# Kernel optimization log

Hardware: AMD Instinct MI355X
Metric: run time of the kernel (lower is better)

Reference implementation:

```python
import jax, jax.numpy as jnp
import numpy as np

NUM_HEADS = 4
C_IN = 80   # in_channels[0] (raw camera BEV channels)
C = 126     # in_channels[1]
D = C + 2   # 128, inner attention dim


def _conv(x, w, b=None):
    # NCHW conv, 3x3, SAME padding (padding=1)
    y = jax.lax.conv_general_dilated(x, w, (1, 1), 'SAME',
                                     dimension_numbers=('NCHW', 'OIHW', 'NCHW'))
    if b is not None:
        y = y + b[None, :, None, None]
    return y


def setup_inputs() -> dict:
    key = jax.random.key(0)
    ks = jax.random.split(key, 16)
    s = 0.02
    inp = {
        'lidar_bev': jax.random.normal(ks[0], (1, C, 64, 64), jnp.float32),
        'cam_bev': jax.random.normal(ks[1], (1, C_IN, 64, 64), jnp.float32),
        'cam_enc_w': jax.random.normal(ks[2], (C, C_IN, 3, 3), jnp.float32) * s,
        'cam_enc_b': jnp.zeros((C,), jnp.float32),
        'cam_v_w': jax.random.normal(ks[3], (D, C), jnp.float32) * s,
        'cam_qk_w': jax.random.normal(ks[4], (2 * D, C), jnp.float32) * s,
        'cam_proj_w': jax.random.normal(ks[5], (C, D), jnp.float32) * s,
        'cam_proj_b': jnp.zeros((C,), jnp.float32),
        'lidar_v_w': jax.random.normal(ks[6], (D, C), jnp.float32) * s,
        'lidar_qk_w': jax.random.normal(ks[7], (2 * D, C), jnp.float32) * s,
        'lidar_proj_w': jax.random.normal(ks[8], (C, D), jnp.float32) * s,
        'lidar_proj_b': jnp.zeros((C,), jnp.float32),
        'fuser_w': jax.random.normal(ks[9], (C, 4 * C, 3, 3), jnp.float32) * s,
    }
    return inp


def reference(lidar_bev, cam_bev, cam_enc_w, cam_enc_b, cam_v_w, cam_qk_w,
              cam_proj_w, cam_proj_b, lidar_v_w, lidar_qk_w, lidar_proj_w,
              lidar_proj_b, fuser_w):
    B, Cc, H, W = lidar_bev.shape
    N = H * W
    nh, hd = NUM_HEADS, D // NUM_HEADS
    scale = Cc ** (-0.5)  # in_channels[1] ** -0.5

    cam_enc = _conv(cam_bev, cam_enc_w, cam_enc_b)  # [B,C,H,W] (SCNET stand-in)

    cam_f = cam_enc.reshape(B, Cc, N).transpose(0, 2, 1)     # [B,N,C]
    lid_f = lidar_bev.reshape(B, Cc, N).transpose(0, 2, 1)    # [B,N,C]

    def heads(x):  # [B,N,D] -> [B,nh,N,hd]
        return x.reshape(B, N, nh, hd).transpose(0, 2, 1, 3)

    cam_v = heads(cam_f @ cam_v_w.T)
    lid_v = heads(lid_f @ lidar_v_w.T)

    def qk(x, w):  # -> (q, k) each [B,nh,N,hd]
        t = (x @ w.T).reshape(B, N, 2, nh, hd).transpose(2, 0, 3, 1, 4)
        return t[0], t[1]

    lid_q, lid_k = qk(lid_f, lidar_qk_w)
    cam_q, cam_k = qk(cam_f, cam_qk_w)

    def merge(o):  # [B,nh,N,hd] -> [B,N,D]
        return o.transpose(0, 2, 1, 3).reshape(B, N, D)

    def to_map(x):  # [B,N,C] -> [B,C,H,W]
        return x.reshape(B, H, W, Cc).transpose(0, 3, 1, 2)

    # lidar-driven attention, reused against two value tensors
    lid_attn = jax.nn.softmax(jnp.einsum('bhnd,bhmd->bhnm', lid_q, lid_k) * scale, axis=-1)
    cam_by_lid = to_map(merge(lid_attn @ cam_v) @ cam_proj_w.T + cam_proj_b)
    cam_bev_l = cam_enc + cam_by_lid
    lid_by_lid = to_map(merge(lid_attn @ lid_v) @ lidar_proj_w.T + lidar_proj_b)
    lidar_bev_l = lidar_bev + lid_by_lid

    # camera-driven attention (note: original code uses lidar_proj for BOTH outputs here)
    cam_attn = jax.nn.softmax(jnp.einsum('bhnd,bhmd->bhnm', cam_q, cam_k) * scale, axis=-1)
    cam_by_cam = to_map(merge(cam_attn @ cam_v) @ lidar_proj_w.T + lidar_proj_b)
    cam_bev_c = cam_enc + cam_by_cam
    lid_by_cam = to_map(merge(cam_attn @ lid_v) @ lidar_proj_w.T + lidar_proj_b)
    lidar_bev_c = lidar_bev + lid_by_cam

    fused_in = jnp.concatenate([cam_bev_c, cam_bev_l, lidar_bev_c, lidar_bev_l], axis=1)
    return _conv(fused_in, fuser_w)
```

## Files before the change

kernel.cpp:

```cpp
#include <hip/hip_runtime.h>
#include <hip/hip_bf16.h>

typedef unsigned short ushort_t;
using f32x4  = __attribute__((ext_vector_type(4))) float;
using f32x16 = __attribute__((ext_vector_type(16))) float;
using bf16x8 = __attribute__((ext_vector_type(8))) short;
typedef unsigned uint2v __attribute__((ext_vector_type(2)));

#define N_PIX 4096

static __device__ __forceinline__ unsigned short f2bf(float f) {
  unsigned int u = __builtin_bit_cast(unsigned int, f);
  u += 0x7FFFu + ((u >> 16) & 1u);
  return (unsigned short)(u >> 16);
}
static __device__ __forceinline__ float bf2f(unsigned int us) {
  return __builtin_bit_cast(float, us << 16);
}

typedef union {
  uint4 u4;
  unsigned u[4];
  unsigned long long q[2];
  bf16x8 v;
  unsigned short us[8];
} fragU;

#define LDS_U32(p) ((unsigned)(uintptr_t)((__attribute__((address_space(3))) void*)(p)))

__global__ __launch_bounds__(256) void zero_span_k(uint4* __restrict__ p, int n16) {
  int i = blockIdx.x * 256 + threadIdx.x;
  if (i < n16) p[i] = (uint4){0u, 0u, 0u, 0u};
}

__global__ __launch_bounds__(256) void prep_k(
    const float* __restrict__ cam_enc_w, const float* __restrict__ fuser_w,
    const float* __restrict__ lid_proj_w, const float* __restrict__ cam_proj_w,
    const float* __restrict__ lid_qk_w, const float* __restrict__ cam_qk_w,
    const float* __restrict__ cam_v_w, const float* __restrict__ lid_v_w,
    const float* __restrict__ cam_bev, const float* __restrict__ lidar_bev,
    ushort_t* __restrict__ Wp_c, ushort_t* __restrict__ Wp_f,
    ushort_t* __restrict__ Wp_lid, ushort_t* __restrict__ Wp_cam,
    ushort_t* __restrict__ Wq,
    ushort_t* __restrict__ cm, ushort_t* __restrict__ ch_,
    ushort_t* __restrict__ lidBF) {
  const float QSCALE = 0.08908708063747479f * 1.4426950408889634f;
  int idx = blockIdx.x * 256 + threadIdx.x;
  if (idx < 110592) {
    int kk = idx / 12288, r = idx % 12288;
    int co = r / 96, ci = r % 96;
    float v = (co < 126 && ci < 80) ? cam_enc_w[(co * 80 + ci) * 9 + kk] : 0.f;
    Wp_c[idx] = f2bf(v);
  } else if (idx < 700416) {
    int j = idx - 110592;
    int kk = j / 65536, r = j % 65536;
    int co = r / 512, ci = r % 512;
    float v = (co < 126 && ci < 504) ? fuser_w[(co * 504 + ci) * 9 + kk] : 0.f;
    Wp_f[j] = f2bf(v);
  } else if (idx < 716800) {
    int j = idx - 700416;
    int co = j >> 7, k = j & 127;
    Wp_lid[j] = f2bf(co < 126 ? lid_proj_w[co * 128 + k] : 0.f);
  } else if (idx < 733184) {
    int j = idx - 716800;
    int co = j >> 7, k = j & 127;
    Wp_cam[j] = f2bf(co < 126 ? cam_proj_w[co * 128 + k] : 0.f);
  } else if (idx < 831488) {
    int j = idx - 733184;
    int t = j >> 14, r = j & 16383;
    int row = r >> 7, ci = r & 127;
    float v = 0.f;
    if (ci < 126) {
      if (t == 0)      v = lid_qk_w[row * 126 + ci] * QSCALE;
      else if (t == 1) v = lid_qk_w[(128 + row) * 126 + ci];
      else if (t == 2) v = cam_qk_w[row * 126 + ci] * QSCALE;
      else if (t == 3) v = cam_qk_w[(128 + row) * 126 + ci];
      else if (t == 4) v = cam_v_w[row * 126 + ci];
      else             v = lid_v_w[row * 126 + ci];
    }
    Wq[j] = f2bf(v);
  } else {
    int k = idx - 831488;
    if (k < 327680) {
      int ch = k >> 12, n = k & 4095;
      int y = n >> 6, x = n & 63;
      unsigned short b = f2bf(cam_bev[k]);
      cm[ch * 4224 + (y + 1) * 64 + x] = b;
      ch_[ch * 4356 + (y + 1) * 66 + (x + 1)] = b;
    } else {
      int j = k - 327680;
      if (j < 516096) lidBF[j] = f2bf(lidar_bev[j]);
    }
  }
}

__global__ __launch_bounds__(256) void conv_mfma_k(
    const ushort_t* __restrict__ Amain,
    const ushort_t* __restrict__ Ahalo,
    const ushort_t* __restrict__ Wp,
    ushort_t* __restrict__ parts,
    int CIp, int ksteps) {
  __shared__ __align__(16) ushort_t Abuf[2][2048];
  const int y   = blockIdx.x;
  const int kk  = blockIdx.y;
  const int ky  = kk / 3, kx = kk - ky * 3;
  const int tid = threadIdx.x;
  const int w   = tid >> 6, l = tid & 63;
  const int lane15 = l & 15, g = l >> 4;
  const int yy1 = y + ky;

  const int ci_l = w * 8 + (l >> 5) * 4 + ((l & 7) >> 1);
  const int m0   = ((l >> 3) & 3) * 16 + (l & 1) * 8;
  const ushort_t* src;
  size_t plane;
  if (kx == 1) { plane = 66 * 64; src = Amain + (size_t)ci_l * plane + yy1 * 64 + m0; }
  else         { plane = 66 * 66; src = Ahalo + (size_t)ci_l * plane + yy1 * 66 + m0 + kx; }

  const ushort_t* wbase = Wp + ((size_t)kk * 128 + w * 32 + lane15) * CIp + g * 8;
  const unsigned tr_base = LDS_U32(&Abuf[0][0]) + (unsigned)(g * 1024 + lane15 * 8);

  f32x4 acc[4][2];
  #pragma unroll
  for (int q = 0; q < 4; ++q) {
    acc[q][0] = (f32x4){0.f, 0.f, 0.f, 0.f};
    acc[q][1] = (f32x4){0.f, 0.f, 0.f, 0.f};
  }

  __builtin_amdgcn_global_load_lds(
      (const __attribute__((address_space(1))) unsigned*)src,
      (__attribute__((address_space(3))) unsigned*)(&Abuf[0][w * 512]), 16, 0, 0);
  __syncthreads();

  for (int s = 0; s < ksteps; ++s) {
    if (s + 1 < ksteps) {
      const ushort_t* srcn = src + (size_t)(s + 1) * 32 * plane;
      __builtin_amdgcn_global_load_lds(
          (const __attribute__((address_space(1))) unsigned*)srcn,
          (__attribute__((address_space(3))) unsigned*)(&Abuf[(s + 1) & 1][w * 512]), 16, 0, 0);
    }
    const ushort_t* wb = wbase + s * 32;
    fragU fb0, fb1;
    fb0.u4 = *(const uint4*)(wb);
    fb1.u4 = *(const uint4*)(wb + 16 * CIp);

    unsigned ta = tr_base + (unsigned)((s & 1) << 12);
    unsigned long long r00, r01, r10, r11, r20, r21, r30, r31;
    asm volatile("ds_read_b64_tr_b16 %0, %1 offset:0"   : "=v"(r00) : "v"(ta));
    asm volatile("ds_read_b64_tr_b16 %0, %1 offset:512" : "=v"(r01) : "v"(ta));
    asm volatile("ds_read_b64_tr_b16 %0, %1 offset:128" : "=v"(r10) : "v"(ta));
    asm volatile("ds_read_b64_tr_b16 %0, %1 offset:640" : "=v"(r11) : "v"(ta));
    asm volatile("ds_read_b64_tr_b16 %0, %1 offset:256" : "=v"(r20) : "v"(ta));
    asm volatile("ds_read_b64_tr_b16 %0, %1 offset:768" : "=v"(r21) : "v"(ta));
    asm volatile("ds_read_b64_tr_b16 %0, %1 offset:384" : "=v"(r30) : "v"(ta));
    asm volatile("ds_read_b64_tr_b16 %0, %1 offset:896" : "=v"(r31) : "v"(ta));
    asm volatile("s_waitcnt lgkmcnt(0)" ::: "memory");
    __builtin_amdgcn_sched_barrier(0);

    fragU fa;
    fa.q[0] = r00; fa.q[1] = r01;
    acc[0][0] = __builtin_amdgcn_mfma_f32_16x16x32_bf16(fa.v, fb0.v, acc[0][0], 0, 0, 0);
    acc[0][1] = __builtin_amdgcn_mfma_f32_16x16x32_bf16(fa.v, fb1.v, acc[0][1], 0, 0, 0);
    fa.q[0] = r10; fa.q[1] = r11;
    acc[1][0] = __builtin_amdgcn_mfma_f32_16x16x32_bf16(fa.v, fb0.v, acc[1][0], 0, 0, 0);
    acc[1][1] = __builtin_amdgcn_mfma_f32_16x16x32_bf16(fa.v, fb1.v, acc[1][1], 0, 0, 0);
    fa.q[0] = r20; fa.q[1] = r21;
    acc[2][0] = __builtin_amdgcn_mfma_f32_16x16x32_bf16(fa.v, fb0.v, acc[2][0], 0, 0, 0);
    acc[2][1] = __builtin_amdgcn_mfma_f32_16x16x32_bf16(fa.v, fb1.v, acc[2][1], 0, 0, 0);
    fa.q[0] = r30; fa.q[1] = r31;
    acc[3][0] = __builtin_amdgcn_mfma_f32_16x16x32_bf16(fa.v, fb0.v, acc[3][0], 0, 0, 0);
    acc[3][1] = __builtin_amdgcn_mfma_f32_16x16x32_bf16(fa.v, fb1.v, acc[3][1], 0, 0, 0);
    __syncthreads();
  }

  ushort_t* pout = parts + (size_t)kk * 524288 + (size_t)(w * 32 + lane15) * 4096
                 + y * 64 + g * 4;
  #pragma unroll
  for (int q = 0; q < 4; ++q) {
    ushort4 p0, p1;
    p0.x = f2bf(acc[q][0][0]); p0.y = f2bf(acc[q][0][1]);
    p0.z = f2bf(acc[q][0][2]); p0.w = f2bf(acc[q][0][3]);
    p1.x = f2bf(acc[q][1][0]); p1.y = f2bf(acc[q][1][1]);
    p1.z = f2bf(acc[q][1][2]); p1.w = f2bf(acc[q][1][3]);
    *(ushort4*)(pout + q * 16)             = p0;
    *(ushort4*)(pout + 16 * 4096 + q * 16) = p1;
  }
}

__global__ __launch_bounds__(256) void reduce9_k(
    const ushort_t* __restrict__ parts, float* __restrict__ out,
    ushort_t* __restrict__ outbf, const float* __restrict__ bias) {
  int n0 = (blockIdx.x * 256 + threadIdx.x) * 8;
  int co = blockIdx.y;
  size_t off = (size_t)co * 4096 + n0;
  float s[8] = {0, 0, 0, 0, 0, 0, 0, 0};
  #pragma unroll
  for (int kk = 0; kk < 9; ++kk) {
    uint4 v = *(const uint4*)(parts + (size_t)kk * 524288 + off);
    s[0] += bf2f(v.x & 0xffffu); s[1] += bf2f(v.x >> 16);
    s[2] += bf2f(v.y & 0xffffu); s[3] += bf2f(v.y >> 16);
    s[4] += bf2f(v.z & 0xffffu); s[5] += bf2f(v.z >> 16);
    s[6] += bf2f(v.w & 0xffffu); s[7] += bf2f(v.w >> 16);
  }
  float b = bias ? bias[co] : 0.f;
  #pragma unroll
  for (int i = 0; i < 8; ++i) s[i] += b;
  if (out) {
    f32x4 o0 = {s[0], s[1], s[2], s[3]};
    f32x4 o1 = {s[4], s[5], s[6], s[7]};
    *(f32x4*)(out + off)     = o0;
    *(f32x4*)(out + off + 4) = o1;
  }
  if (outbf) {
    ushort4 b0, b1;
    b0.x = f2bf(s[0]); b0.y = f2bf(s[1]); b0.z = f2bf(s[2]); b0.w = f2bf(s[3]);
    b1.x = f2bf(s[4]); b1.y = f2bf(s[5]); b1.z = f2bf(s[6]); b1.w = f2bf(s[7]);
    *(ushort4*)(outbf + off)     = b0;
    *(ushort4*)(outbf + off + 4) = b1;
  }
}

__global__ __launch_bounds__(256) void qkv_mfma_k(
    const ushort_t* __restrict__ lidBF, const ushort_t* __restrict__ camBF,
    const ushort_t* __restrict__ Wq,
    ushort_t* __restrict__ lidQK, ushort_t* __restrict__ camQK,
    ushort_t* __restrict__ camV, ushort_t* __restrict__ lidV) {
  __shared__ __align__(16) ushort_t Abuf[2][2048];
  const int y = blockIdx.x, t = blockIdx.y;
  const ushort_t* X = (t >= 2 && t <= 4) ? camBF : lidBF;
  const int tid = threadIdx.x;
  const int w = tid >> 6, l = tid & 63;
  const int lane15 = l & 15, g = l >> 4;
  const int ci_l = w * 8 + (l >> 5) * 4 + ((l & 7) >> 1);
  const int m0   = ((l >> 3) & 3) * 16 + (l & 1) * 8;
  const ushort_t* src = X + (size_t)ci_l * 4096 + y * 64 + m0;
  const ushort_t* wbase = Wq + (size_t)t * 16384 + (w * 32 + lane15) * 128 + g * 8;
  const unsigned tr_base = LDS_U32(&Abuf[0][0]) + (unsigned)(g * 1024 + lane15 * 8);

  f32x4 acc[4][2];
  #pragma unroll
  for (int q = 0; q < 4; ++q) {
    acc[q][0] = (f32x4){0.f, 0.f, 0.f, 0.f};
    acc[q][1] = (f32x4){0.f, 0.f, 0.f, 0.f};
  }

  __builtin_amdgcn_global_load_lds(
      (const __attribute__((address_space(1))) unsigned*)src,
      (__attribute__((address_space(3))) unsigned*)(&Abuf[0][w * 512]), 16, 0, 0);
  __syncthreads();

  for (int s = 0; s < 4; ++s) {
    if (s < 3) {
      const ushort_t* srcn = src + (size_t)(s + 1) * 32 * 4096;
      __builtin_amdgcn_global_load_lds(
          (const __attribute__((address_space(1))) unsigned*)srcn,
          (__attribute__((address_space(3))) unsigned*)(&Abuf[(s + 1) & 1][w * 512]), 16, 0, 0);
    }
    const ushort_t* wb = wbase + s * 32;
    fragU fb0, fb1;
    fb0.u4 = *(const uint4*)(wb);
    fb1.u4 = *(const uint4*)(wb + 16 * 128);

    unsigned ta = tr_base + (unsigned)((s & 1) << 12);
    unsigned long long r00, r01, r10, r11, r20, r21, r30, r31;
    asm volatile("ds_read_b64_tr_b16 %0, %1 offset:0"   : "=v"(r00) : "v"(ta));
    asm volatile("ds_read_b64_tr_b16 %0, %1 offset:512" : "=v"(r01) : "v"(ta));
    asm volatile("ds_read_b64_tr_b16 %0, %1 offset:128" : "=v"(r10) : "v"(ta));
    asm volatile("ds_read_b64_tr_b16 %0, %1 offset:640" : "=v"(r11) : "v"(ta));
    asm volatile("ds_read_b64_tr_b16 %0, %1 offset:256" : "=v"(r20) : "v"(ta));
    asm volatile("ds_read_b64_tr_b16 %0, %1 offset:768" : "=v"(r21) : "v"(ta));
    asm volatile("ds_read_b64_tr_b16 %0, %1 offset:384" : "=v"(r30) : "v"(ta));
    asm volatile("ds_read_b64_tr_b16 %0, %1 offset:896" : "=v"(r31) : "v"(ta));
    asm volatile("s_waitcnt lgkmcnt(0)" ::: "memory");
    __builtin_amdgcn_sched_barrier(0);

    fragU fa;
    fa.q[0] = r00; fa.q[1] = r01;
    acc[0][0] = __builtin_amdgcn_mfma_f32_16x16x32_bf16(fa.v, fb0.v, acc[0][0], 0, 0, 0);
    acc[0][1] = __builtin_amdgcn_mfma_f32_16x16x32_bf16(fa.v, fb1.v, acc[0][1], 0, 0, 0);
    fa.q[0] = r10; fa.q[1] = r11;
    acc[1][0] = __builtin_amdgcn_mfma_f32_16x16x32_bf16(fa.v, fb0.v, acc[1][0], 0, 0, 0);
    acc[1][1] = __builtin_amdgcn_mfma_f32_16x16x32_bf16(fa.v, fb1.v, acc[1][1], 0, 0, 0);
    fa.q[0] = r20; fa.q[1] = r21;
    acc[2][0] = __builtin_amdgcn_mfma_f32_16x16x32_bf16(fa.v, fb0.v, acc[2][0], 0, 0, 0);
    acc[2][1] = __builtin_amdgcn_mfma_f32_16x16x32_bf16(fa.v, fb1.v, acc[2][1], 0, 0, 0);
    fa.q[0] = r30; fa.q[1] = r31;
    acc[3][0] = __builtin_amdgcn_mfma_f32_16x16x32_bf16(fa.v, fb0.v, acc[3][0], 0, 0, 0);
    acc[3][1] = __builtin_amdgcn_mfma_f32_16x16x32_bf16(fa.v, fb1.v, acc[3][1], 0, 0, 0);
    __syncthreads();
  }

  if (t < 4) {
    ushort_t* dst = (t < 2) ? lidQK : camQK;
    const int colbase = (t & 1) * 128 + w * 32 + lane15;
    #pragma unroll
    for (int q = 0; q < 4; ++q)
      #pragma unroll
      for (int tt = 0; tt < 2; ++tt)
        #pragma unroll
        for (int r = 0; r < 4; ++r) {
          int n = y * 64 + q * 16 + g * 4 + r;
          dst[(size_t)n * 256 + colbase + tt * 16] = f2bf(acc[q][tt][r]);
        }
  } else {
    ushort_t* dst = (t == 4) ? camV : lidV;
    ushort_t* pout = dst + (size_t)(w * 32 + lane15) * 4096 + y * 64 + g * 4;
    #pragma unroll
    for (int q = 0; q < 4; ++q) {
      ushort4 p0, p1;
      p0.x = f2bf(acc[q][0][0]); p0.y = f2bf(acc[q][0][1]);
      p0.z = f2bf(acc[q][0][2]); p0.w = f2bf(acc[q][0][3]);
      p1.x = f2bf(acc[q][1][0]); p1.y = f2bf(acc[q][1][1]);
      p1.z = f2bf(acc[q][1][2]); p1.w = f2bf(acc[q][1][3]);
      *(ushort4*)(pout + q * 16)             = p0;
      *(ushort4*)(pout + 16 * 4096 + q * 16) = p1;
    }
  }
}

__global__ __launch_bounds__(256) void flash_attn_mfma(
    const ushort_t* __restrict__ lidQK, const ushort_t* __restrict__ camQK,
    const ushort_t* __restrict__ camV, const ushort_t* __restrict__ lidV,
    ushort_t* __restrict__ OP, float2* __restrict__ ML) {
  const int i0    = blockIdx.x * 128;
  const int h     = blockIdx.y;
  const int attn  = blockIdx.z >> 1;
  const int half  = blockIdx.z & 1;
  const int kbase = half * 2048;
  const ushort_t* QK = attn ? camQK : lidQK;

  __shared__ __align__(16) ushort_t Ks[2][64 * 40];
  __shared__ __align__(16) ushort_t Vt[2][64 * 72];

  const int tid = threadIdx.x;
  const int w = tid >> 6, l = tid & 63;
  const int q31 = l & 31, hi = l >> 5;
  const int q0w = i0 + w * 32;

  const int srow = tid >> 2, sc = tid & 3;
  const ushort_t* Kg = QK + (size_t)(kbase + srow) * 256 + 128 + h * 32 + sc * 8;
  const ushort_t* Vg = ((srow >> 5) ? lidV : camV)
                     + (size_t)(h * 32 + (srow & 31)) * N_PIX + kbase;

  fragU qf0, qf1;
  qf0.u4 = *(const uint4*)(QK + (size_t)(q0w + q31) * 256 + h * 32 + hi * 8);
  qf1.u4 = *(const uint4*)(QK + (size_t)(q0w + q31) * 256 + h * 32 + 16 + hi * 8);

  {
    uint4 k4 = *(const uint4*)Kg;
    uint4 va = *(const uint4*)(Vg + sc * 8);
    uint4 vb = *(const uint4*)(Vg + (sc + 4) * 8);
    *(uint4*)(&Ks[0][srow * 40 + sc * 8]) = k4;
    *(uint4*)(&Vt[0][srow * 72 + sc * 8]) = va;
    *(uint4*)(&Vt[0][srow * 72 + (sc + 4) * 8]) = vb;
  }
  __syncthreads();

  fragU ones;
  #pragma unroll
  for (int j = 0; j < 8; ++j) ones.us[j] = 0x3F80;

  f32x16 Oc = (f32x16)0.f, Ol = (f32x16)0.f, lacc = (f32x16)0.f;
  const f32x16 z16 = (f32x16)0.f;

  for (int it = 0; it < 32; ++it) {
    const int cur = it & 1, nxt = cur ^ 1;
    const bool more = (it + 1) < 32;
    uint4 kn, van, vbn;
    if (more) {
      kn  = *(const uint4*)(Kg + (size_t)(it + 1) * 16384);
      van = *(const uint4*)(Vg + (it + 1) * 64 + sc * 8);
      vbn = *(const uint4*)(Vg + (it + 1) * 64 + (sc + 4) * 8);
    }

    const ushort_t* kb = &Ks[cur][0];
    fragU k00, k01, k10, k11;
    k00.u4 = *(const uint4*)(kb + q31 * 40 + hi * 8);
    k01.u4 = *(const uint4*)(kb + q31 * 40 + 16 + hi * 8);
    k10.u4 = *(const uint4*)(kb + (32 + q31) * 40 + hi * 8);
    k11.u4 = *(const uint4*)(kb + (32 + q31) * 40 + 16 + hi * 8);
    f32x16 S0, S1;
    __builtin_amdgcn_s_setprio(1);
    S0 = __builtin_amdgcn_mfma_f32_32x32x16_bf16(k00.v, qf0.v, z16, 0, 0, 0);
    S0 = __builtin_amdgcn_mfma_f32_32x32x16_bf16(k01.v, qf1.v, S0, 0, 0, 0);
    S1 = __builtin_amdgcn_mfma_f32_32x32x16_bf16(k10.v, qf0.v, z16, 0, 0, 0);
    S1 = __builtin_amdgcn_mfma_f32_32x32x16_bf16(k11.v, qf1.v, S1, 0, 0, 0);
    __builtin_amdgcn_s_setprio(0);

    #pragma unroll
    for (int j = 0; j < 16; ++j) S0[j] = __builtin_amdgcn_exp2f(S0[j]);
    #pragma unroll
    for (int j = 0; j < 16; ++j) S1[j] = __builtin_amdgcn_exp2f(S1[j]);

    fragU pa0, pa1, pa2, pa3;
    {
      unsigned a0, a1, b0, b1;
      asm("v_cvt_pk_bf16_f32 %0, %1, %2" : "=v"(a0) : "v"(S0[0]),  "v"(S0[1]));
      asm("v_cvt_pk_bf16_f32 %0, %1, %2" : "=v"(a1) : "v"(S0[2]),  "v"(S0[3]));
      asm("v_cvt_pk_bf16_f32 %0, %1, %2" : "=v"(b0) : "v"(S0[4]),  "v"(S0[5]));
      asm("v_cvt_pk_bf16_f32 %0, %1, %2" : "=v"(b1) : "v"(S0[6]),  "v"(S0[7]));
      uint2v r0 = __builtin_amdgcn_permlane32_swap(a0, b0, false, false);
      uint2v r1 = __builtin_amdgcn_permlane32_swap(a1, b1, false, false);
      pa0.u[0] = r0[0]; pa0.u[1] = r1[0]; pa0.u[2] = r0[1]; pa0.u[3] = r1[1];
      asm("v_cvt_pk_bf16_f32 %0, %1, %2" : "=v"(a0) : "v"(S0[8]),  "v"(S0[9]));
      asm("v_cvt_pk_bf16_f32 %0, %1, %2" : "=v"(a1) : "v"(S0[10]), "v"(S0[11]));
      asm("v_cvt_pk_bf16_f32 %0, %1, %2" : "=v"(b0) : "v"(S0[12]), "v"(S0[13]));
      asm("v_cvt_pk_bf16_f32 %0, %1, %2" : "=v"(b1) : "v"(S0[14]), "v"(S0[15]));
      r0 = __builtin_amdgcn_permlane32_swap(a0, b0, false, false);
      r1 = __builtin_amdgcn_permlane32_swap(a1, b1, false, false);
      pa1.u[0] = r0[0]; pa1.u[1] = r1[0]; pa1.u[2] = r0[1]; pa1.u[3] = r1[1];
      asm("v_cvt_pk_bf16_f32 %0, %1, %2" : "=v"(a0) : "v"(S1[0]),  "v"(S1[1]));
      asm("v_cvt_pk_bf16_f32 %0, %1, %2" : "=v"(a1) : "v"(S1[2]),  "v"(S1[3]));
      asm("v_cvt_pk_bf16_f32 %0, %1, %2" : "=v"(b0) : "v"(S1[4]),  "v"(S1[5]));
      asm("v_cvt_pk_bf16_f32 %0, %1, %2" : "=v"(b1) : "v"(S1[6]),  "v"(S1[7]));
      r0 = __builtin_amdgcn_permlane32_swap(a0, b0, false, false);
      r1 = __builtin_amdgcn_permlane32_swap(a1, b1, false, false);
      pa2.u[0] = r0[0]; pa2.u[1] = r1[0]; pa2.u[2] = r0[1]; pa2.u[3] = r1[1];
      asm("v_cvt_pk_bf16_f32 %0, %1, %2" : "=v"(a0) : "v"(S1[8]),  "v"(S1[9]));
      asm("v_cvt_pk_bf16_f32 %0, %1, %2" : "=v"(a1) : "v"(S1[10]), "v"(S1[11]));
      asm("v_cvt_pk_bf16_f32 %0, %1, %2" : "=v"(b0) : "v"(S1[12]), "v"(S1[13]));
      asm("v_cvt_pk_bf16_f32 %0, %1, %2" : "=v"(b1) : "v"(S1[14]), "v"(S1[15]));
      r0 = __builtin_amdgcn_permlane32_swap(a0, b0, false, false);
      r1 = __builtin_amdgcn_permlane32_swap(a1, b1, false, false);
      pa3.u[0] = r0[0]; pa3.u[1] = r1[0]; pa3.u[2] = r0[1]; pa3.u[3] = r1[1];
    }

    const ushort_t* vb = &Vt[cur][0];
    __builtin_amdgcn_s_setprio(1);
    {
      fragU vc, vl;
      vc.u4 = *(const uint4*)(vb + q31 * 72 + hi * 8);
      vl.u4 = *(const uint4*)(vb + (32 + q31) * 72 + hi * 8);
      Oc = __builtin_amdgcn_mfma_f32_32x32x16_bf16(pa0.v, vc.v, Oc, 0, 0, 0);
      Ol = __builtin_amdgcn_mfma_f32_32x32x16_bf16(pa0.v, vl.v, Ol, 0, 0, 0);
      lacc = __builtin_amdgcn_mfma_f32_32x32x16_bf16(pa0.v, ones.v, lacc, 0, 0, 0);
      vc.u4 = *(const uint4*)(vb + q31 * 72 + 16 + hi * 8);
      vl.u4 = *(const uint4*)(vb + (32 + q31) * 72 + 16 + hi * 8);
      Oc = __builtin_amdgcn_mfma_f32_32x32x16_bf16(pa1.v, vc.v, Oc, 0, 0, 0);
      Ol = __builtin_amdgcn_mfma_f32_32x32x16_bf16(pa1.v, vl.v, Ol, 0, 0, 0);
      lacc = __builtin_amdgcn_mfma_f32_32x32x16_bf16(pa1.v, ones.v, lacc, 0, 0, 0);
      vc.u4 = *(const uint4*)(vb + q31 * 72 + 32 + hi * 8);
      vl.u4 = *(const uint4*)(vb + (32 + q31) * 72 + 32 + hi * 8);
      Oc = __builtin_amdgcn_mfma_f32_32x32x16_bf16(pa2.v, vc.v, Oc, 0, 0, 0);
      Ol = __builtin_amdgcn_mfma_f32_32x32x16_bf16(pa2.v, vl.v, Ol, 0, 0, 0);
      lacc = __builtin_amdgcn_mfma_f32_32x32x16_bf16(pa2.v, ones.v, lacc, 0, 0, 0);
      vc.u4 = *(const uint4*)(vb + q31 * 72 + 48 + hi * 8);
      vl.u4 = *(const uint4*)(vb + (32 + q31) * 72 + 48 + hi * 8);
      Oc = __builtin_amdgcn_mfma_f32_32x32x16_bf16(pa3.v, vc.v, Oc, 0, 0, 0);
      Ol = __builtin_amdgcn_mfma_f32_32x32x16_bf16(pa3.v, vl.v, Ol, 0, 0, 0);
      lacc = __builtin_amdgcn_mfma_f32_32x32x16_bf16(pa3.v, ones.v, lacc, 0, 0, 0);
    }
    __builtin_amdgcn_s_setprio(0);

    if (more) {
      *(uint4*)(&Ks[nxt][srow * 40 + sc * 8]) = kn;
      *(uint4*)(&Vt[nxt][srow * 72 + sc * 8]) = van;
      *(uint4*)(&Vt[nxt][srow * 72 + (sc + 4) * 8]) = vbn;
    }
    __syncthreads();
  }

  ushort_t* OPc = OP + (size_t)((attn * 2 + half) * 2 + 0) * 4096 * 128;
  ushort_t* OPl = OP + (size_t)((attn * 2 + half) * 2 + 1) * 4096 * 128;
  const int d = h * 32 + q31;
  #pragma unroll
  for (int reg = 0; reg < 16; ++reg) {
    int n = q0w + (reg & 3) + 8 * (reg >> 2) + 4 * hi;
    OPc[(size_t)n * 128 + d] = f2bf(Oc[reg]);
    OPl[(size_t)n * 128 + d] = f2bf(Ol[reg]);
  }
  if (q31 == 0) {
    #pragma unroll
    for (int reg = 0; reg < 16; ++reg) {
      int n = q0w + (reg & 3) + 8 * (reg >> 2) + 4 * hi;
      float2 v; v.x = 0.f; v.y = lacc[reg];
      ML[(size_t)(attn * 2 + half) * 4096 + n] = v;
    }
  }
}

__global__ __launch_bounds__(256) void proj_mfma_k(
    const ushort_t* __restrict__ OP, const float2* __restrict__ ML,
    const ushort_t* __restrict__ Wlid, const ushort_t* __restrict__ Wcam,
    const ushort_t* __restrict__ camBF, const ushort_t* __restrict__ lidBF,
    const float* __restrict__ cam_proj_b, const float* __restrict__ lid_proj_b,
    ushort_t* __restrict__ fm, ushort_t* __restrict__ fh) {
  const int n0 = blockIdx.x * 64;
  const int ot = blockIdx.y;
  const int attn = (ot == 0 || ot == 2) ? 1 : 0;
  const int vt = ot >> 1;
  const int tid = threadIdx.x;
  const int w = tid >> 6, l = tid & 63;
  const int m = l & 15, g = l >> 4;

  const ushort_t* Oa = OP + (size_t)((attn * 2 + 0) * 2 + vt) * 4096 * 128;
  const ushort_t* Ob = OP + (size_t)((attn * 2 + 1) * 2 + vt) * 4096 * 128;
  const float2* MLa = ML + (size_t)(attn * 2 + 0) * 4096;
  const float2* MLb = ML + (size_t)(attn * 2 + 1) * 4096;

  const int arow = n0 + w * 16 + m;
  float2 mla = MLa[arow], mlb = MLb[arow];
  float inv = 1.0f / (mla.y + mlb.y);

  fragU afr[4];
  #pragma unroll
  for (int s = 0; s < 4; ++s) {
    fragU xa, xb;
    xa.u4 = *(const uint4*)(Oa + (size_t)arow * 128 + s * 32 + g * 8);
    xb.u4 = *(const uint4*)(Ob + (size_t)arow * 128 + s * 32 + g * 8);
    #pragma unroll
    for (int j = 0; j < 8; ++j)
      afr[s].us[j] = f2bf(inv * (bf2f(xa.us[j]) + bf2f(xb.us[j])));
  }

  const ushort_t* W = (ot == 1) ? Wcam : Wlid;
  f32x4 acc[8];
  #pragma unroll
  for (int t = 0; t < 8; ++t) acc[t] = (f32x4){0.f, 0.f, 0.f, 0.f};
  #pragma unroll
  for (int s = 0; s < 4; ++s) {
    #pragma unroll
    for (int t = 0; t < 8; ++t) {
      fragU bfr;
      bfr.u4 = *(const uint4*)(W + (size_t)(t * 16 + m) * 128 + s * 32 + g * 8);
      acc[t] = __builtin_amdgcn_mfma_f32_16x16x32_bf16(afr[s].v, bfr.v, acc[t], 0, 0, 0);
    }
  }

  const float* bias = (ot == 1) ? cam_proj_b : lid_proj_b;
  const ushort_t* resBF = (ot < 2) ? camBF : lidBF;
  const int doff = ot * 126;
  #pragma unroll
  for (int t = 0; t < 8; ++t) {
    int co = t * 16 + m;
    if (co < 126) {
      float b = bias[co];
      #pragma unroll
      for (int r = 0; r < 4; ++r) {
        int n = n0 + w * 16 + g * 4 + r;
        float res = bf2f(resBF[(size_t)co * N_PIX + n]);
        float v = acc[t][r] + res + b;
        unsigned short bf = f2bf(v);
        int y = n >> 6, x = n & 63;
        fm[(doff + co) * 4224 + (y + 1) * 64 + x]      = bf;
        fh[(doff + co) * 4356 + (y + 1) * 66 + x + 1]  = bf;
      }
    }
  }
}

extern "C" void kernel_launch(void* const* d_in, const int* in_sizes, int n_in,
                              void* d_out, int out_size, void* d_ws, size_t ws_size,
                              hipStream_t stream) {
  (void)in_sizes; (void)n_in; (void)out_size; (void)ws_size;
  const float* lidar_bev  = (const float*)d_in[0];
  const float* cam_bev    = (const float*)d_in[1];
  const float* cam_enc_w  = (const float*)d_in[2];
  const float* cam_enc_b  = (const float*)d_in[3];
  const float* cam_v_w    = (const float*)d_in[4];
  const float* cam_qk_w   = (const float*)d_in[5];
  const float* cam_proj_w = (const float*)d_in[6];
  const float* cam_proj_b = (const float*)d_in[7];
  const float* lid_v_w    = (const float*)d_in[8];
  const float* lid_qk_w   = (const float*)d_in[9];
  const float* lid_proj_w = (const float*)d_in[10];
  const float* lid_proj_b = (const float*)d_in[11];
  const float* fuser_w    = (const float*)d_in[12];
  float* out = (float*)d_out;

  char* p = (char*)d_ws;
  ushort_t* arena = (ushort_t*)p;
  ushort_t* OP    = (ushort_t*)p;
  float2*   ML    = (float2*)(p + 8388608);
  ushort_t* lidQK = (ushort_t*)(p + 9437184);
  ushort_t* camQK = (ushort_t*)(p + 11534336);
  ushort_t* camV  = (ushort_t*)(p + 13631488);
  ushort_t* lidV  = (ushort_t*)(p + 14680064);
  ushort_t* Wp_c    = (ushort_t*)(p + 17793024);
  ushort_t* Wp_f    = (ushort_t*)(p + 18014208);
  ushort_t* Wp_lid  = (ushort_t*)(p + 19193856);
  ushort_t* Wp_cam  = (ushort_t*)(p + 19226624);
  ushort_t* Wq      = (ushort_t*)(p + 19259392);
  ushort_t* lidBF   = (ushort_t*)(p + 19456000);
  ushort_t* camBF   = (ushort_t*)(p + 20504576);
  ushort_t* camBF_m = (ushort_t*)(p + 21553152);
  ushort_t* camBF_h = (ushort_t*)(p + 22364160);
  ushort_t* fusBF_m = (ushort_t*)(p + 23200512);
  ushort_t* fusBF_h = (ushort_t*)(p + 27525888);

  zero_span_k<<<2548, 256, 0, stream>>>((uint4*)(p + 21553152), 652080);
  prep_k<<<6544, 256, 0, stream>>>(cam_enc_w, fuser_w, lid_proj_w, cam_proj_w,
                                   lid_qk_w, cam_qk_w, cam_v_w, lid_v_w,
                                   cam_bev, lidar_bev,
                                   Wp_c, Wp_f, Wp_lid, Wp_cam, Wq,
                                   camBF_m, camBF_h, lidBF);

  conv_mfma_k<<<dim3(64, 9), 256, 0, stream>>>(camBF_m, camBF_h, Wp_c, arena, 96, 3);
  reduce9_k<<<dim3(2, 126), 256, 0, stream>>>(arena, nullptr, camBF, cam_enc_b);

  qkv_mfma_k<<<dim3(64, 6), 256, 0, stream>>>(lidBF, camBF, Wq, lidQK, camQK, camV, lidV);
  flash_attn_mfma<<<dim3(32, 4, 4), 256, 0, stream>>>(lidQK, camQK, camV, lidV, OP, ML);
  proj_mfma_k<<<dim3(64, 4), 256, 0, stream>>>(OP, ML, Wp_lid, Wp_cam, camBF, lidBF,
                                               cam_proj_b, lid_proj_b, fusBF_m, fusBF_h);

  conv_mfma_k<<<dim3(64, 9), 256, 0, stream>>>(fusBF_m, fusBF_h, Wp_f, arena, 512, 16);
  reduce9_k<<<dim3(2, 126), 256, 0, stream>>>(arena, out, nullptr, nullptr);
}
```

Before: 114.1 us.

## Split attention key range four ways to double flash-attention grid parallelism

The flash attention kernel now splits the key dimension into four chunks instead of two, launching 1024 blocks instead of 512, each iterating half as many key tiles. Partial outputs are placed in workspace regions that overlap the fuser-input buffers, so zeroing of that span is moved to after attention, and the projection kernel sums four partials and four row sums. This aims to raise CU occupancy on the attention stage, at the cost of extra partial-output traffic, a second zeroing launch, and more reduction work in the projection.

```diff
diff --git a/kernel.cpp b/kernel.cpp
--- a/kernel.cpp
+++ b/kernel.cpp
@@ -27,6 +27,11 @@
 } fragU;
 
 #define LDS_U32(p) ((unsigned)(uintptr_t)((__attribute__((address_space(3))) void*)(p)))
+
+static __device__ __forceinline__ size_t op_off(int s) {
+  return (s < 9) ? ((size_t)s << 20) : ((size_t)23200512u + ((size_t)(s - 9) << 20));
+}
+#define ML_OFF 15728640u
 
 __global__ __launch_bounds__(256) void zero_span_k(uint4* __restrict__ p, int n16) {
   int i = blockIdx.x * 256 + threadIdx.x;
@@ -320,12 +325,13 @@
 __global__ __launch_bounds__(256) void flash_attn_mfma(
     const ushort_t* __restrict__ lidQK, const ushort_t* __restrict__ camQK,
     const ushort_t* __restrict__ camV, const ushort_t* __restrict__ lidV,
-    ushort_t* __restrict__ OP, float2* __restrict__ ML) {
+    char* __restrict__ ws) {
   const int i0    = blockIdx.x * 128;
   const int h     = blockIdx.y;
-  const int attn  = blockIdx.z >> 1;
-  const int half  = blockIdx.z & 1;
-  const int kbase = half * 2048;
+  const int z     = blockIdx.z;
+  const int attn  = z >> 2;
+  const int split = z & 3;
+  const int kbase = split * 1024;
   const ushort_t* QK = attn ? camQK : lidQK;
 
   __shared__ __align__(16) ushort_t Ks[2][64 * 40];
@@ -362,9 +368,9 @@
   f32x16 Oc = (f32x16)0.f, Ol = (f32x16)0.f, lacc = (f32x16)0.f;
   const f32x16 z16 = (f32x16)0.f;
 
-  for (int it = 0; it < 32; ++it) {
+  for (int it = 0; it < 16; ++it) {
     const int cur = it & 1, nxt = cur ^ 1;
-    const bool more = (it + 1) < 32;
+    const bool more = (it + 1) < 16;
     uint4 kn, van, vbn;
     if (more) {
       kn  = *(const uint4*)(Kg + (size_t)(it + 1) * 16384);
@@ -459,8 +465,10 @@
     __syncthreads();
   }
 
-  ushort_t* OPc = OP + (size_t)((attn * 2 + half) * 2 + 0) * 4096 * 128;
-  ushort_t* OPl = OP + (size_t)((attn * 2 + half) * 2 + 1) * 4096 * 128;
+  const int si = (attn * 4 + split) * 2;
+  ushort_t* OPc = (ushort_t*)(ws + op_off(si + 0));
+  ushort_t* OPl = (ushort_t*)(ws + op_off(si + 1));
+  float2* ML = (float2*)(ws + ML_OFF);
   const int d = h * 32 + q31;
   #pragma unroll
   for (int reg = 0; reg < 16; ++reg) {
@@ -473,13 +481,13 @@
     for (int reg = 0; reg < 16; ++reg) {
       int n = q0w + (reg & 3) + 8 * (reg >> 2) + 4 * hi;
       float2 v; v.x = 0.f; v.y = lacc[reg];
-      ML[(size_t)(attn * 2 + half) * 4096 + n] = v;
+      ML[(size_t)(attn * 4 + split) * 4096 + n] = v;
     }
   }
 }
 
 __global__ __launch_bounds__(256) void proj_mfma_k(
-    const ushort_t* __restrict__ OP, const float2* __restrict__ ML,
+    const char* __restrict__ ws,
     const ushort_t* __restrict__ Wlid, const ushort_t* __restrict__ Wcam,
     const ushort_t* __restrict__ camBF, const ushort_t* __restrict__ lidBF,
     const float* __restrict__ cam_proj_b, const float* __restrict__ lid_proj_b,
@@ -492,24 +500,32 @@
   const int w = tid >> 6, l = tid & 63;
   const int m = l & 15, g = l >> 4;
 
-  const ushort_t* Oa = OP + (size_t)((attn * 2 + 0) * 2 + vt) * 4096 * 128;
-  const ushort_t* Ob = OP + (size_t)((attn * 2 + 1) * 2 + vt) * 4096 * 128;
-  const float2* MLa = ML + (size_t)(attn * 2 + 0) * 4096;
-  const float2* MLb = ML + (size_t)(attn * 2 + 1) * 4096;
-
+  const float2* ML = (const float2*)(ws + ML_OFF);
   const int arow = n0 + w * 16 + m;
-  float2 mla = MLa[arow], mlb = MLb[arow];
-  float inv = 1.0f / (mla.y + mlb.y);
+
+  float lsum = 0.f;
+  #pragma unroll
+  for (int s = 0; s < 4; ++s)
+    lsum += ML[(size_t)(attn * 4 + s) * 4096 + arow].y;
+  float inv = 1.0f / lsum;
+
+  const ushort_t* O0 = (const ushort_t*)(ws + op_off((attn * 4 + 0) * 2 + vt));
+  const ushort_t* O1 = (const ushort_t*)(ws + op_off((attn * 4 + 1) * 2 + vt));
+  const ushort_t* O2 = (const ushort_t*)(ws + op_off((attn * 4 + 2) * 2 + vt));
+  const ushort_t* O3 = (const ushort_t*)(ws + op_off((attn * 4 + 3) * 2 + vt));
 
   fragU afr[4];
   #pragma unroll
   for (int s = 0; s < 4; ++s) {
-    fragU xa, xb;
-    xa.u4 = *(const uint4*)(Oa + (size_t)arow * 128 + s * 32 + g * 8);
-    xb.u4 = *(const uint4*)(Ob + (size_t)arow * 128 + s * 32 + g * 8);
+    fragU x0, x1, x2, x3;
+    x0.u4 = *(const uint4*)(O0 + (size_t)arow * 128 + s * 32 + g * 8);
+    x1.u4 = *(const uint4*)(O1 + (size_t)arow * 128 + s * 32 + g * 8);
+    x2.u4 = *(const uint4*)(O2 + (size_t)arow * 128 + s * 32 + g * 8);
+    x3.u4 = *(const uint4*)(O3 + (size_t)arow * 128 + s * 32 + g * 8);
     #pragma unroll
     for (int j = 0; j < 8; ++j)
-      afr[s].us[j] = f2bf(inv * (bf2f(xa.us[j]) + bf2f(xb.us[j])));
+      afr[s].us[j] = f2bf(inv * (bf2f(x0.us[j]) + bf2f(x1.us[j])
+                               + bf2f(x2.us[j]) + bf2f(x3.us[j])));
   }
 
   const ushort_t* W = (ot == 1) ? Wcam : Wlid;
@@ -569,8 +585,6 @@
 
   char* p = (char*)d_ws;
   ushort_t* arena = (ushort_t*)p;
-  ushort_t* OP    = (ushort_t*)p;
-  float2*   ML    = (float2*)(p + 8388608);
   ushort_t* lidQK = (ushort_t*)(p + 9437184);
   ushort_t* camQK = (ushort_t*)(p + 11534336);
   ushort_t* camV  = (ushort_t*)(p + 13631488);
@@ -587,7 +601,7 @@
   ushort_t* fusBF_m = (ushort_t*)(p + 23200512);
   ushort_t* fusBF_h = (ushort_t*)(p + 27525888);
 
-  zero_span_k<<<2548, 256, 0, stream>>>((uint4*)(p + 21553152), 652080);
+  zero_span_k<<<403, 256, 0, stream>>>((uint4*)(p + 21553152), 102960);
   prep_k<<<6544, 256, 0, stream>>>(cam_enc_w, fuser_w, lid_proj_w, cam_proj_w,
                                    lid_qk_w, cam_qk_w, cam_v_w, lid_v_w,
                                    cam_bev, lidar_bev,
@@ -598,8 +612,9 @@
   reduce9_k<<<dim3(2, 126), 256, 0, stream>>>(arena, nullptr, camBF, cam_enc_b);
 
   qkv_mfma_k<<<dim3(64, 6), 256, 0, stream>>>(lidBF, camBF, Wq, lidQK, camQK, camV, lidV);
-  flash_attn_mfma<<<dim3(32, 4, 4), 256, 0, stream>>>(lidQK, camQK, camV, lidV, OP, ML);
-  proj_mfma_k<<<dim3(64, 4), 256, 0, stream>>>(OP, ML, Wp_lid, Wp_cam, camBF, lidBF,
+  flash_attn_mfma<<<dim3(32, 4, 8), 256, 0, stream>>>(lidQK, camQK, camV, lidV, p);
+  zero_span_k<<<2145, 256, 0, stream>>>((uint4*)(p + 23200512), 549120);
+  proj_mfma_k<<<dim3(64, 4), 256, 0, stream>>>(p, Wp_lid, Wp_cam, camBF, lidBF,
                                                cam_proj_b, lid_proj_b, fusBF_m, fusBF_h);
 
   conv_mfma_k<<<dim3(64, 9), 256, 0, stream>>>(fusBF_m, fusBF_h, Wp_f, arena, 512, 16);
```

Measured after the change: 116.7 us. 1.02x slower.
